# Kernel optimization log

Measured on AMD Instinct MI355X. Metric: run time of the kernel, lower is better.

Reference implementation:

```python
import jax, jax.numpy as jnp
import numpy as np

DIM = 384
HEADS = 12
WIN = (2, 7, 7)
MLP_RATIO = 4.0
EPS = 1e-5


def _rel_index(Wt, Wh, Ww):
    t, h, w = np.meshgrid(np.arange(Wt), np.arange(Wh), np.arange(Ww), indexing='ij')
    coords = np.stack([t, h, w]).reshape(3, -1).T  # (N,3)
    rel = coords[:, None] - coords[None]  # (N,N,3)
    rel[..., 0] += Wt - 1
    rel[..., 1] += Wh - 1
    rel[..., 2] += Ww - 1
    rel[..., 0] *= (2 * Wh - 1) * (2 * Ww - 1)
    rel[..., 1] *= (2 * Ww - 1)
    return rel.sum(-1)  # (N,N) int


def setup_inputs() -> dict:
    key = jax.random.key(0)
    ks = jax.random.split(key, 16)
    d = DIM
    hdim = int(d * MLP_RATIO)
    Wt, Wh, Ww = WIN
    table_size = (2 * Wt - 1) * (2 * Wh - 1) * (2 * Ww - 1)
    s = lambda fan: 1.0 / np.sqrt(fan)
    return {
        'x': jax.random.normal(ks[0], (2, 8, 56, 56, d), jnp.float32),
        'norm1_g': jnp.ones((d,), jnp.float32),
        'norm1_b': jnp.zeros((d,), jnp.float32),
        'qkv_w': jax.random.normal(ks[1], (d, 3 * d), jnp.float32) * s(d),
        'qkv_b': jnp.zeros((3 * d,), jnp.float32),
        'proj_w': jax.random.normal(ks[2], (d, d), jnp.float32) * s(d),
        'proj_b': jnp.zeros((d,), jnp.float32),
        'bias_table': jax.random.normal(ks[3], (table_size, HEADS), jnp.float32) * 0.02,
        'norm2_g': jnp.ones((d,), jnp.float32),
        'norm2_b': jnp.zeros((d,), jnp.float32),
        'fc1_w': jax.random.normal(ks[4], (d, hdim), jnp.float32) * s(d),
        'fc1_b': jnp.zeros((hdim,), jnp.float32),
        'fc2_w': jax.random.normal(ks[5], (hdim, d), jnp.float32) * s(hdim),
        'fc2_b': jnp.zeros((d,), jnp.float32),
        'rel_index': jnp.asarray(_rel_index(*WIN), jnp.int32),
    }


def _ln(x, g, b):
    mu = x.mean(-1, keepdims=True)
    var = ((x - mu) ** 2).mean(-1, keepdims=True)
    return (x - mu) * jax.lax.rsqrt(var + EPS) * g + b


def _window_partition(x, win):
    B, T, H, W, C = x.shape
    Wt, Wh, Ww = win
    x = x.reshape(B, T // Wt, Wt, H // Wh, Wh, W // Ww, Ww, C)
    x = x.transpose(0, 1, 3, 5, 2, 4, 6, 7)
    return x.reshape(-1, Wt * Wh * Ww, C)


def _window_reverse(win_x, win, B, T, H, W):
    Wt, Wh, Ww = win
    C = win_x.shape[-1]
    x = win_x.reshape(B, T // Wt, H // Wh, W // Ww, Wt, Wh, Ww, C)
    x = x.transpose(0, 1, 4, 2, 5, 3, 6, 7)
    return x.reshape(B, T, H, W, C)


def reference(x, norm1_g, norm1_b, qkv_w, qkv_b, proj_w, proj_b, bias_table,
              norm2_g, norm2_b, fc1_w, fc1_b, fc2_w, fc2_b, rel_index):
    B, T, H, W, C = x.shape
    Wt, Wh, Ww = WIN
    N = Wt * Wh * Ww
    shift = (Wt // 2, Wh // 2, Ww // 2)
    head_dim = C // HEADS
    scale = head_dim ** -0.5

    shortcut = x
    h = _ln(x, norm1_g, norm1_b)
    h = jnp.roll(h, shift=(-shift[0], -shift[1], -shift[2]), axis=(1, 2, 3))
    # dims chosen divisible by window -> no padding branch
    wins = _window_partition(h, WIN)  # (BnW, N, C)
    BnW = wins.shape[0]

    qkv = wins @ qkv_w + qkv_b  # (BnW, N, 3C)
    qkv = qkv.reshape(BnW, N, 3, HEADS, head_dim).transpose(2, 0, 3, 1, 4)
    q, k, v = qkv[0] * scale, qkv[1], qkv[2]  # (BnW, H, N, d)

    bias = bias_table[rel_index.reshape(-1)].reshape(N, N, HEADS).transpose(2, 0, 1)
    attn = jnp.einsum('bhnd,bhmd->bhnm', q, k) + bias[None]
    attn = jax.nn.softmax(attn, axis=-1)
    out = jnp.einsum('bhnm,bhmd->bhnd', attn, v)
    out = out.transpose(0, 2, 1, 3).reshape(BnW, N, C)
    out = out @ proj_w + proj_b

    h = _window_reverse(out.reshape(-1, Wt, Wh, Ww, C), WIN, B, T, H, W)
    h = jnp.roll(h, shift=shift, axis=(1, 2, 3))
    x = shortcut + h

    h2 = _ln(x, norm2_g, norm2_b)
    h2 = jax.nn.gelu(h2 @ fc1_w + fc1_b, approximate=False) @ fc2_w + fc2_b
    return x + h2
```

## Files before the change

kernel.cpp:

```cpp
#include <hip/hip_runtime.h>
#include <cstdint>
#include <cstddef>


typedef __bf16 bf16x8 __attribute__((ext_vector_type(8)));
typedef __bf16 bf16x4 __attribute__((ext_vector_type(4)));
typedef float f32x4 __attribute__((ext_vector_type(4)));

#define DIM 384
#define QKV_DIM 1152
#define HID 1536
#define NHEADS 12
#define NTOK 50176
#define NWIN 512

__device__ __forceinline__ void gload16(const void* g, void* s) {
  __builtin_amdgcn_global_load_lds(
      (const __attribute__((address_space(1))) void*)g,
      (__attribute__((address_space(3))) void*)s, 16, 0, 0);
}

__global__ __launch_bounds__(256) void build_tokmap_k(int* __restrict__ map) {
  int t = blockIdx.x * 256 + threadIdx.x;
  if (t >= NTOK) return;
  int win = t / 98, n = t - win * 98;
  int b = win >> 8, tw = (win >> 6) & 3, hw = (win >> 3) & 7, ww = win & 7;
  int dt = n / 49; int rem = n - dt * 49; int dh = rem / 7, dw = rem - dh * 7;
  int t0 = (tw * 2 + dt + 1) & 7;
  int h0 = hw * 7 + dh + 3; if (h0 >= 56) h0 -= 56;
  int w0 = ww * 7 + dw + 3; if (w0 >= 56) w0 -= 56;
  map[t] = ((b * 8 + t0) * 56 + h0) * 56 + w0;
}

__global__ __launch_bounds__(256) void expand_biasp_k(const float* __restrict__ table,
                                                      const int* __restrict__ rel,
                                                      float* __restrict__ out) {
  int e = blockIdx.x * 256 + threadIdx.x;
  if (e >= NHEADS * 49 * 256) return;
  int r = e & 3, l = (e >> 2) & 63;
  int rest = e >> 8;
  int ni = rest % 7, mi = (rest / 7) % 7, h = rest / 49;
  int i = mi * 16 + (l >> 4) * 4 + r;
  int j = ni * 16 + (l & 15);
  float v;
  if (j >= 98) v = -1e30f;
  else if (i >= 98) v = 0.f;
  else v = table[rel[i * 98 + j] * NHEADS + h];
  out[e] = v;
}

__global__ __launch_bounds__(256) void pack_w64_k(const float* __restrict__ W,
                                                  __bf16* __restrict__ WP,
                                                  int K, int N, int nk,
                                                  int scaleCols, float scale) {
  int idx = blockIdx.x * 256 + threadIdx.x;
  if (idx >= (K * N) >> 3) return;
  int l = idx & 63, f = (idx >> 6) & 7;
  int rest = idx >> 9, kt = rest % nk, cn = rest / nk;
  int n = f >> 1, kk = f & 1;
  int col = cn * 64 + n * 16 + (l & 15);
  int k0 = kt * 64 + (kk * 4 + (l >> 4)) * 8;
  float sc = (col < scaleCols) ? scale : 1.0f;
  bf16x8 v;
  #pragma unroll
  for (int j = 0; j < 8; ++j)
    v[j] = (__bf16)(W[(size_t)(k0 + j) * N + col] * sc);
  *(bf16x8*)(WP + (size_t)idx * 8) = v;
}

__global__ __launch_bounds__(256) void scale_bias_k(const float* __restrict__ b,
                                                    float* __restrict__ out,
                                                    int n, int scaleCols, float scale) {
  int e = blockIdx.x * 256 + threadIdx.x;
  if (e >= n) return;
  out[e] = b[e] * (e < scaleCols ? scale : 1.0f);
}

__global__ __launch_bounds__(384) void vtrans_k(const __bf16* __restrict__ qkv,
                                                __bf16* __restrict__ vt) {
  __shared__ __align__(1024) char T[98304];
  int win = blockIdx.x, t = threadIdx.x;
  const __bf16* base = qkv + (size_t)win * 98 * QKV_DIM + 768 + t;
  #pragma unroll
  for (int c = 0; c < 16; ++c) {
    bf16x8 pk;
    #pragma unroll
    for (int e2 = 0; e2 < 8; ++e2) {
      int tok = c * 8 + e2;
      pk[e2] = (tok < 98) ? base[(size_t)tok * QKV_DIM] : (__bf16)0.f;
    }
    *(bf16x8*)(T + t * 256 + ((c ^ (t & 15)) << 4)) = pk;
  }
  __syncthreads();
  char* wb = (char*)(vt + (size_t)win * 49152);
  #pragma unroll
  for (int i = 0; i < 16; ++i) {
    int g = i * 6144 + t * 16;
    int row = g >> 8, p = (g >> 4) & 15;
    bf16x8 v = *(const bf16x8*)(T + row * 256 + (p << 4));
    int lc = p ^ (row & 15);
    *(bf16x8*)(wb + row * 256 + (lc << 4)) = v;
  }
}

template <typename T, bool MAP>
__global__ __launch_bounds__(256) void ln_pack_k(const T* __restrict__ x,
                                                 const float* __restrict__ g,
                                                 const float* __restrict__ bta,
                                                 __bf16* __restrict__ outp,
                                                 const int* __restrict__ map) {
  const int w = threadIdx.x >> 6, l = threadIdx.x & 63;
  const int tok = blockIdx.x * 32 + w * 8 + (l >> 3);
  const int src = MAP ? map[tok] : tok;
  const T* row = x + (size_t)src * DIM;
  const int o0 = l & 7;
  float v[6][8];
  float s = 0.f;
  #pragma unroll
  for (int j = 0; j < 6; ++j) {
    const int c = (o0 + 8 * j) * 8;
    if constexpr (sizeof(T) == 4) {
      f32x4 p0 = *(const f32x4*)(row + c);
      f32x4 p1 = *(const f32x4*)(row + c + 4);
      #pragma unroll
      for (int e = 0; e < 4; ++e) { v[j][e] = p0[e]; v[j][e + 4] = p1[e]; }
    } else {
      bf16x8 p = *(const bf16x8*)(row + c);
      #pragma unroll
      for (int e = 0; e < 8; ++e) v[j][e] = (float)p[e];
    }
    #pragma unroll
    for (int e = 0; e < 8; ++e) s += v[j][e];
  }
  s += __shfl_xor(s, 1, 64); s += __shfl_xor(s, 2, 64); s += __shfl_xor(s, 4, 64);
  const float mu = s * (1.f / DIM);
  float var = 0.f;
  #pragma unroll
  for (int j = 0; j < 6; ++j)
    #pragma unroll
    for (int e = 0; e < 8; ++e) { float d = v[j][e] - mu; var += d * d; }
  var += __shfl_xor(var, 1, 64); var += __shfl_xor(var, 2, 64); var += __shfl_xor(var, 4, 64);
  const float rs = rsqrtf(var * (1.f / DIM) + 1e-5f);
  const int mg = tok >> 6, m = (tok >> 4) & 3, lr = tok & 15;
  const int kk = o0 >> 2, lg = o0 & 3;
  __bf16* dst = outp + (size_t)mg * 24576 + (m * 2 + kk) * 512 + (lg * 16 + lr) * 8;
  #pragma unroll
  for (int j = 0; j < 6; ++j) {
    const int c = (o0 + 8 * j) * 8;
    f32x4 g0 = *(const f32x4*)(g + c), g1 = *(const f32x4*)(g + c + 4);
    f32x4 b0 = *(const f32x4*)(bta + c), b1 = *(const f32x4*)(bta + c + 4);
    bf16x8 ov;
    #pragma unroll
    for (int e = 0; e < 4; ++e) {
      ov[e] = (__bf16)((v[j][e] - mu) * rs * g0[e] + b0[e]);
      ov[e + 4] = (__bf16)((v[j][e + 4] - mu) * rs * g1[e] + b1[e]);
    }
    *(bf16x8*)(dst + (size_t)j * 4096) = ov;
  }
}

template <int EPI, int NK>
__global__ __launch_bounds__(256) void gemm_stream_k(const __bf16* __restrict__ AP,
                                                     const __bf16* __restrict__ WP,
                                                     const float* __restrict__ bias,
                                                     int N,
                                                     __bf16* __restrict__ outb,
                                                     float* __restrict__ outf,
                                                     const __bf16* __restrict__ residb) {
  __shared__ __align__(1024) char lds[32768];
  const int tid = threadIdx.x;
  const int l = tid & 63, w = tid >> 6;
  const int lr = l & 15, lg = l >> 4;
  const int ntile = N >> 6;
  const int nwg = gridDim.x, qd = nwg >> 3, rm = nwg & 7;
  const int xcd = blockIdx.x & 7;
  const int wgid = (xcd < rm ? xcd * (qd + 1) : rm * (qd + 1) + (xcd - rm) * qd)
                   + (blockIdx.x >> 3);
  const int bm = wgid / ntile, bn = wgid - bm * ntile;
  const int mg = bm * 4 + w;
  const int m0 = mg << 6, n0 = bn << 6;
  const __bf16* pA = AP + (size_t)mg * (NK * 4096) + l * 8;
  const __bf16* pB = WP + (size_t)bn * (NK * 4096) + l * 8;

  bf16x8 a[2][8], b[2][8];
  f32x4 acc[4][4] = {};
  #pragma unroll
  for (int f = 0; f < 8; ++f) {
    a[0][f] = *(const bf16x8*)(pA + f * 512);
    b[0][f] = *(const bf16x8*)(pB + f * 512);
  }
  #pragma unroll
  for (int kt = 0; kt < NK; ++kt) {
    const int cur = kt & 1, nxt = cur ^ 1;
    if (kt < NK - 1) {
      const size_t ko = (size_t)(kt + 1) * 4096;
      #pragma unroll
      for (int f = 0; f < 8; ++f) {
        a[nxt][f] = *(const bf16x8*)(pA + ko + f * 512);
        b[nxt][f] = *(const bf16x8*)(pB + ko + f * 512);
      }
      asm volatile("s_waitcnt vmcnt(16)" ::: "memory");
    } else {
      asm volatile("s_waitcnt vmcnt(0)" ::: "memory");
    }
    __builtin_amdgcn_sched_barrier(0);
    __builtin_amdgcn_s_setprio(1);
    #pragma unroll
    for (int kk = 0; kk < 2; ++kk)
      #pragma unroll
      for (int m = 0; m < 4; ++m)
        #pragma unroll
        for (int n = 0; n < 4; ++n)
          acc[m][n] = __builtin_amdgcn_mfma_f32_16x16x32_bf16(
              b[cur][n * 2 + kk], a[cur][m * 2 + kk], acc[m][n], 0, 0, 0);
    __builtin_amdgcn_s_setprio(0);
  }

  char* abuf = lds + (w << 13);
  if (EPI == 3) {
    #pragma unroll
    for (int hh = 0; hh < 2; ++hh) {
      #pragma unroll
      for (int m = 0; m < 4; ++m) {
        const int row = (m << 4) + lr;
        #pragma unroll
        for (int n2 = 0; n2 < 2; ++n2) {
          const int n = (hh << 1) + n2;
          const int gcol = n0 + (n << 4) + (lg << 2);
          f32x4 a4 = acc[m][n] + *(const f32x4*)(bias + gcol);
          const int ch = (n2 << 2) + lg;
          *(f32x4*)(abuf + (row << 7) + ((ch ^ (row & 7)) << 4)) = a4;
        }
      }
      asm volatile("s_waitcnt lgkmcnt(0)" ::: "memory");
      __builtin_amdgcn_sched_barrier(0);
      #pragma unroll
      for (int i = 0; i < 8; ++i) {
        const int row = (i << 3) + (l >> 3);
        const int p = (l & 7) ^ (row & 7);
        f32x4 v = *(const f32x4*)(abuf + (row << 7) + (p << 4));
        const int grow = m0 + row;
        const int gcol = n0 + (hh << 5) + ((l & 7) << 2);
        bf16x4 sv = *(const bf16x4*)(residb + (size_t)grow * N + gcol);
        f32x4 o;
        #pragma unroll
        for (int r = 0; r < 4; ++r) o[r] = v[r] + (float)sv[r];
        *(f32x4*)(outf + (size_t)grow * N + gcol) = o;
      }
      if (hh == 0) {
        asm volatile("s_waitcnt lgkmcnt(0)" ::: "memory");
        __builtin_amdgcn_sched_barrier(0);
      }
    }
  } else {
    #pragma unroll
    for (int m = 0; m < 4; ++m) {
      const int row = (m << 4) + lr;
      #pragma unroll
      for (int n = 0; n < 4; ++n) {
        const int gcol = n0 + (n << 4) + (lg << 2);
        f32x4 a4 = acc[m][n] + *(const f32x4*)(bias + gcol);
        bf16x4 c;
        if (EPI == 4) {
          #pragma unroll
          for (int r = 0; r < 4; ++r) {
            float vv = a4[r];
            float y = vv * (1.0f + 0.044715f * vv * vv);
            c[r] = (__bf16)(vv / (1.0f + __expf(-1.5957691216057308f * y)));
          }
        } else {
          #pragma unroll
          for (int r = 0; r < 4; ++r) c[r] = (__bf16)a4[r];
        }
        const int ch = (n << 1) + (lg >> 1);
        *(bf16x4*)(abuf + (row << 7) + ((ch ^ (row & 7)) << 4) + ((lg & 1) << 3)) = c;
      }
    }
    asm volatile("s_waitcnt lgkmcnt(0)" ::: "memory");
    __builtin_amdgcn_sched_barrier(0);
    if (EPI == 4) {
      #pragma unroll
      for (int f = 0; f < 8; ++f) {
        const int row = ((f >> 1) << 4) + lr;
        const int lc = ((f & 1) << 2) + (l >> 4);
        const int ph = lc ^ (row & 7);
        bf16x8 v = *(const bf16x8*)(abuf + (row << 7) + (ph << 4));
        *(bf16x8*)(outb + ((size_t)(mg * 24 + bn) * 8 + f) * 512 + l * 8) = v;
      }
    } else {
      #pragma unroll
      for (int i = 0; i < 8; ++i) {
        const int row = (i << 3) + (l >> 3);
        const int p = (l & 7) ^ (row & 7);
        bf16x8 v = *(const bf16x8*)(abuf + (row << 7) + (p << 4));
        *(bf16x8*)(outb + (size_t)(m0 + row) * N + n0 + ((l & 7) << 3)) = v;
      }
    }
  }
}

__global__ __launch_bounds__(256) void gemm_proj_k(const __bf16* __restrict__ A,
                                                   const __bf16* __restrict__ WP,
                                                   const float* __restrict__ bias,
                                                   int M, int N, int K,
                                                   __bf16* __restrict__ outb,
                                                   const float* __restrict__ residf,
                                                   const int* __restrict__ tokmap) {
  __shared__ __align__(1024) char lds[32768];
  const int tid = threadIdx.x;
  const int l = tid & 63, w = tid >> 6;
  const int lr = l & 15, lg = l >> 4;
  const int ntile = N >> 6;
  const int nwg = gridDim.x, qd = nwg >> 3, rm = nwg & 7;
  const int xcd = blockIdx.x & 7;
  const int wgid = (xcd < rm ? xcd * (qd + 1) : rm * (qd + 1) + (xcd - rm) * qd)
                   + (blockIdx.x >> 3);
  const int bm = wgid / ntile, bn = wgid - bm * ntile;
  const int m0 = (bm << 8) + (w << 6);
  const int n0 = bn << 6;
  const int nk = K >> 6;
  const int sch = (l & 7) ^ ((l >> 3) & 7);
  const __bf16* pa = A + (size_t)(m0 + (l >> 3)) * K + sch * 8;
  char* abuf = lds + (w << 13);
  const __bf16* pB = WP + (size_t)bn * nk * 4096 + l * 8;

#define STAGEA(kt)                                                   \
  { const size_t ko_ = (size_t)(kt) << 6;                            \
    _Pragma("unroll")                                                \
    for (int s_ = 0; s_ < 8; ++s_)                                   \
      gload16(pa + (size_t)(s_ * 8) * K + ko_, abuf + s_ * 1024); }
#define LOADB(kt)                                                    \
  { const __bf16* p_ = pB + (size_t)(kt) * 4096;                     \
    _Pragma("unroll")                                                \
    for (int f_ = 0; f_ < 8; ++f_)                                   \
      b[f_] = *(const bf16x8*)(p_ + f_ * 512); }
#define LDA()                                                        \
  { _Pragma("unroll")                                                \
    for (int kk_ = 0; kk_ < 2; ++kk_) {                              \
      const int ck_ = (kk_ << 2) + lg;                               \
      _Pragma("unroll")                                              \
      for (int m_ = 0; m_ < 4; ++m_) {                               \
        int r_ = (m_ << 4) + lr;                                     \
        a[m_][kk_] = *(const bf16x8*)(abuf + (r_ << 7) +             \
                                      ((ck_ ^ (r_ & 7)) << 4));      \
      } }                                                            \
    asm volatile("s_waitcnt lgkmcnt(0)" ::: "memory");               \
    __builtin_amdgcn_sched_barrier(0); }

  bf16x8 a[4][2], b[8];
  f32x4 acc[4][4] = {};
  STAGEA(0)
  asm volatile("s_waitcnt vmcnt(0)" ::: "memory");
  LDA()
  for (int kt = 0; kt < nk; ++kt) {
    LOADB(kt)
    const bool pf = (kt + 1 < nk);
    if (pf) STAGEA(kt + 1)
    __builtin_amdgcn_s_setprio(1);
    #pragma unroll
    for (int kk = 0; kk < 2; ++kk)
      #pragma unroll
      for (int m = 0; m < 4; ++m)
        #pragma unroll
        for (int n = 0; n < 4; ++n)
          acc[m][n] = __builtin_amdgcn_mfma_f32_16x16x32_bf16(b[n * 2 + kk], a[m][kk],
                                                              acc[m][n], 0, 0, 0);
    __builtin_amdgcn_s_setprio(0);
    if (pf) {
      asm volatile("s_waitcnt vmcnt(0)" ::: "memory");
      LDA()
    }
  }
#undef STAGEA
#undef LOADB
#undef LDA

  #pragma unroll
  for (int m = 0; m < 4; ++m) {
    const int row = (m << 4) + lr;
    #pragma unroll
    for (int n = 0; n < 4; ++n) {
      const int gcol = n0 + (n << 4) + (lg << 2);
      f32x4 a4 = acc[m][n] + *(const f32x4*)(bias + gcol);
      bf16x4 c;
      #pragma unroll
      for (int r = 0; r < 4; ++r) c[r] = (__bf16)a4[r];
      const int ch = (n << 1) + (lg >> 1);
      *(bf16x4*)(abuf + (row << 7) + ((ch ^ (row & 7)) << 4) + ((lg & 1) << 3)) = c;
    }
  }
  asm volatile("s_waitcnt lgkmcnt(0)" ::: "memory");
  __builtin_amdgcn_sched_barrier(0);
  #pragma unroll
  for (int i = 0; i < 8; ++i) {
    const int row = (i << 3) + (l >> 3);
    const int p = (l & 7) ^ (row & 7);
    bf16x8 v = *(const bf16x8*)(abuf + (row << 7) + (p << 4));
    const int gcol = n0 + ((l & 7) << 3);
    const int dst = tokmap[m0 + row];
    const float* rp = residf + (size_t)dst * N + gcol;
    f32x4 r0 = *(const f32x4*)rp, r1 = *(const f32x4*)(rp + 4);
    bf16x8 c2;
    #pragma unroll
    for (int j = 0; j < 4; ++j) {
      c2[j] = (__bf16)(r0[j] + (float)v[j]);
      c2[j + 4] = (__bf16)(r1[j] + (float)v[j + 4]);
    }
    *(bf16x8*)(outb + (size_t)dst * N + gcol) = c2;
  }
}

__global__ __launch_bounds__(64) void attn_k(const __bf16* __restrict__ qkv,
                                             const __bf16* __restrict__ vt,
                                             const float* __restrict__ pb,
                                             __bf16* __restrict__ out) {
  __shared__ __align__(1024) char P[4096];
  const int l = threadIdx.x, lr = l & 15, lg = l >> 4;
  const int bid = blockIdx.x;
  const int xc = bid & 7, kk = bid >> 3;
  const int wh = (kk / 7) * 8 + xc, mi = kk % 7;
  const int win = wh / NHEADS, h = wh - win * NHEADS;
  const size_t wbase = (size_t)win * 98 * QKV_DIM;
  const __bf16* qb = qkv + wbase + h * 32;
  const __bf16* kb = qb + 384;
  const bf16x8 z8 = {};
  const f32x4 fz = {};

  bf16x8 kf[7];
  #pragma unroll
  for (int ni = 0; ni < 7; ++ni) {
    int tok = ni * 16 + lr;
    kf[ni] = (tok < 98) ? *(const bf16x8*)(kb + (size_t)tok * QKV_DIM + lg * 8) : z8;
  }
  int qt = mi * 16 + lr;
  bf16x8 qf = (qt < 98) ? *(const bf16x8*)(qb + (size_t)qt * QKV_DIM + lg * 8) : z8;
  const f32x4* pbp = (const f32x4*)pb + (size_t)((h * 7 + mi) * 7) * 64 + l;
  f32x4 bv[7];
  #pragma unroll
  for (int ni = 0; ni < 7; ++ni) bv[ni] = pbp[ni * 64];

  f32x4 s[7];
  #pragma unroll
  for (int ni = 0; ni < 7; ++ni)
    s[ni] = __builtin_amdgcn_mfma_f32_16x16x32_bf16(qf, kf[ni], fz, 0, 0, 0);

  if (l < 32) {
    int row = l >> 1, c = 14 + (l & 1);
    *(f32x4*)(P + row * 256 + ((c ^ (row & 7)) << 4)) = fz;
  }

  #pragma unroll
  for (int r = 0; r < 4; ++r) {
    float mx = -1e30f;
    #pragma unroll
    for (int ni = 0; ni < 7; ++ni) {
      float vv = s[ni][r] + bv[ni][r];
      s[ni][r] = vv;
      mx = fmaxf(mx, vv);
    }
    #pragma unroll
    for (int m2 = 1; m2 < 16; m2 <<= 1) mx = fmaxf(mx, __shfl_xor(mx, m2, 64));
    float sum = 0.f;
    #pragma unroll
    for (int ni = 0; ni < 7; ++ni) { float p = __expf(s[ni][r] - mx); s[ni][r] = p; sum += p; }
    #pragma unroll
    for (int m2 = 1; m2 < 16; m2 <<= 1) sum += __shfl_xor(sum, m2, 64);
    float inv = 1.0f / sum;
    int il = lg * 4 + r;
    #pragma unroll
    for (int ni = 0; ni < 7; ++ni) {
      int j = ni * 16 + lr;
      *(__bf16*)(P + il * 256 + (((j >> 3) ^ (il & 7)) << 4) + ((j & 7) << 1)) =
          (__bf16)(s[ni][r] * inv);
    }
  }
  __syncthreads();

  bf16x8 pa[4];
  #pragma unroll
  for (int ks = 0; ks < 4; ++ks) {
    int ck = ks * 4 + lg;
    pa[ks] = *(const bf16x8*)(P + lr * 256 + ((ck ^ (lr & 7)) << 4));
  }
  const __bf16* vrow = vt + ((size_t)wh * 32) * 128;
  f32x4 oo[2];
  #pragma unroll
  for (int nf = 0; nf < 2; ++nf) {
    int d = nf * 16 + lr;
    f32x4 o = fz;
    #pragma unroll
    for (int ks = 0; ks < 4; ++ks) {
      bf16x8 vb = *(const bf16x8*)(vrow + (size_t)d * 128 + ks * 32 + lg * 8);
      o = __builtin_amdgcn_mfma_f32_16x16x32_bf16(pa[ks], vb, o, 0, 0, 0);
    }
    oo[nf] = o;
  }
  #pragma unroll
  for (int nf = 0; nf < 2; ++nf)
    #pragma unroll
    for (int r = 0; r < 4; ++r)
      *(__bf16*)(P + (lg * 4 + r) * 64 + (((nf << 4) + lr) << 1)) = (__bf16)oo[nf][r];
  asm volatile("s_waitcnt lgkmcnt(0)" ::: "memory");
  __builtin_amdgcn_sched_barrier(0);
  {
    const int row = l >> 2;
    bf16x8 v = *(const bf16x8*)(P + row * 64 + ((l & 3) << 4));
    const int tok = mi * 16 + row;
    if (tok < 98)
      *(bf16x8*)(out + ((size_t)win * 98 + tok) * DIM + h * 32 + ((l & 3) << 3)) = v;
  }
}

extern "C" void kernel_launch(void* const* d_in, const int* in_sizes, int n_in,
                              void* d_out, int out_size, void* d_ws, size_t ws_size,
                              hipStream_t stream) {
  const float* x      = (const float*)d_in[0];
  const float* n1g    = (const float*)d_in[1];
  const float* n1b    = (const float*)d_in[2];
  const float* qkv_w  = (const float*)d_in[3];
  const float* qkv_b  = (const float*)d_in[4];
  const float* proj_w = (const float*)d_in[5];
  const float* proj_b = (const float*)d_in[6];
  const float* btab   = (const float*)d_in[7];
  const float* n2g    = (const float*)d_in[8];
  const float* n2b    = (const float*)d_in[9];
  const float* fc1_w  = (const float*)d_in[10];
  const float* fc1_b  = (const float*)d_in[11];
  const float* fc2_w  = (const float*)d_in[12];
  const float* fc2_b  = (const float*)d_in[13];
  const int*   relidx = (const int*)d_in[14];
  float* outp = (float*)d_out;
  (void)in_sizes; (void)n_in; (void)out_size; (void)ws_size;

  char* ws = (char*)d_ws;
  size_t off = 0;
  auto alloc = [&](size_t bytes) {
    char* p = ws + off;
    off = (off + bytes + 255) & ~(size_t)255;
    return p;
  };
  int*    tokmap  = (int*)alloc((size_t)NTOK * 4);
  float*  biasex  = (float*)alloc((size_t)NHEADS * 49 * 256 * 4);
  __bf16* wqkvP   = (__bf16*)alloc((size_t)QKV_DIM * DIM * 2);
  __bf16* wprojP  = (__bf16*)alloc((size_t)DIM * DIM * 2);
  __bf16* wfc1P   = (__bf16*)alloc((size_t)HID * DIM * 2);
  __bf16* wfc2P   = (__bf16*)alloc((size_t)DIM * HID * 2);
  float*  qkvbS   = (float*)alloc((size_t)QKV_DIM * 4);
  __bf16* tokens  = (__bf16*)alloc((size_t)NTOK * DIM * 2);
  __bf16* qkvbuf  = (__bf16*)alloc((size_t)NTOK * HID * 2);
  __bf16* s1      = (__bf16*)alloc((size_t)NTOK * DIM * 2);
  __bf16* tokens2 = (__bf16*)alloc((size_t)NTOK * DIM * 2);
  __bf16* attnout = tokens;
  __bf16* h1P = qkvbuf;
  __bf16* vt = (__bf16*)d_out;

  const float scale = 0.17677669529663687f;

  build_tokmap_k<<<NTOK / 256, 256, 0, stream>>>(tokmap);
  expand_biasp_k<<<(NHEADS * 49 * 256) / 256, 256, 0, stream>>>(btab, relidx, biasex);
  pack_w64_k<<<(DIM * QKV_DIM / 8) / 256, 256, 0, stream>>>(qkv_w, wqkvP, DIM, QKV_DIM, 6, DIM, scale);
  pack_w64_k<<<(DIM * DIM / 8) / 256, 256, 0, stream>>>(proj_w, wprojP, DIM, DIM, 6, 0, 1.0f);
  pack_w64_k<<<(DIM * HID / 8) / 256, 256, 0, stream>>>(fc1_w, wfc1P, DIM, HID, 6, 0, 1.0f);
  pack_w64_k<<<(HID * DIM / 8) / 256, 256, 0, stream>>>(fc2_w, wfc2P, HID, DIM, 24, 0, 1.0f);
  scale_bias_k<<<(QKV_DIM + 255) / 256, 256, 0, stream>>>(qkv_b, qkvbS, QKV_DIM, DIM, scale);

  ln_pack_k<float, true><<<NTOK / 32, 256, 0, stream>>>(x, n1g, n1b, tokens, tokmap);
  gemm_stream_k<0, 6><<<(NTOK / 256) * (QKV_DIM / 64), 256, 0, stream>>>(
      tokens, wqkvP, qkvbS, QKV_DIM, qkvbuf, nullptr, nullptr);
  vtrans_k<<<NWIN, 384, 0, stream>>>(qkvbuf, vt);
  attn_k<<<NWIN * NHEADS * 7, 64, 0, stream>>>(qkvbuf, vt, biasex, attnout);
  gemm_proj_k<<<(NTOK / 256) * (DIM / 64), 256, 0, stream>>>(
      attnout, wprojP, proj_b, NTOK, DIM, DIM, s1, x, tokmap);
  ln_pack_k<__bf16, false><<<NTOK / 32, 256, 0, stream>>>(s1, n2g, n2b, tokens2, nullptr);
  gemm_stream_k<4, 6><<<(NTOK / 256) * (HID / 64), 256, 0, stream>>>(
      tokens2, wfc1P, fc1_b, HID, h1P, nullptr, nullptr);
  gemm_stream_k<3, 24><<<(NTOK / 256) * (DIM / 64), 256, 0, stream>>>(
      h1P, wfc2P, fc2_b, DIM, nullptr, outp, s1);
}
```

Baseline: 455.2 us.

## Fuse fc1, GELU and fc2 into one MLP kernel keeping hidden activations in LDS

Replaces the separate fc1 (with GELU) and fc2 GEMM launches with one kernel per 64-token tile. The kernel loads the normalized tokens into LDS, computes fc1 chunks with GELU into LDS, and accumulates fc2 directly in registers, then adds bias and the residual. The fc2 weights are repacked in a new 96-column layout to match. This removes the round trip of the large hidden activation through global memory. In exchange, weights are read from global memory per tile without LDS staging, the tile is small, and barriers plus higher register and LDS use limit occupancy.

```diff
diff --git a/kernel.cpp b/kernel.cpp
--- a/kernel.cpp
+++ b/kernel.cpp
@@ -68,6 +68,21 @@
   *(bf16x8*)(WP + (size_t)idx * 8) = v;
 }
 
+__global__ __launch_bounds__(256) void pack_w96_k(const float* __restrict__ W,
+                                                  __bf16* __restrict__ WP) {
+  int idx = blockIdx.x * 256 + threadIdx.x;
+  if (idx >= (HID * DIM) >> 3) return;
+  int l = idx & 63, n = (idx >> 6) % 6;
+  int j8 = (idx / 384) % 48, w = idx / 18432;
+  int col = w * 96 + n * 16 + (l & 15);
+  int k0 = j8 * 32 + (l >> 4) * 8;
+  bf16x8 v;
+  #pragma unroll
+  for (int j = 0; j < 8; ++j)
+    v[j] = (__bf16)W[(size_t)(k0 + j) * DIM + col];
+  *(bf16x8*)(WP + (size_t)idx * 8) = v;
+}
+
 __global__ __launch_bounds__(256) void scale_bias_k(const float* __restrict__ b,
                                                     float* __restrict__ out,
                                                     int n, int scaleCols, float scale) {
@@ -164,9 +179,7 @@
                                                      const __bf16* __restrict__ WP,
                                                      const float* __restrict__ bias,
                                                      int N,
-                                                     __bf16* __restrict__ outb,
-                                                     float* __restrict__ outf,
-                                                     const __bf16* __restrict__ residb) {
+                                                     __bf16* __restrict__ outb) {
   __shared__ __align__(1024) char lds[32768];
   const int tid = threadIdx.x;
   const int l = tid & 63, w = tid >> 6;
@@ -217,84 +230,149 @@
   }
 
   char* abuf = lds + (w << 13);
-  if (EPI == 3) {
-    #pragma unroll
-    for (int hh = 0; hh < 2; ++hh) {
-      #pragma unroll
-      for (int m = 0; m < 4; ++m) {
-        const int row = (m << 4) + lr;
-        #pragma unroll
-        for (int n2 = 0; n2 < 2; ++n2) {
-          const int n = (hh << 1) + n2;
-          const int gcol = n0 + (n << 4) + (lg << 2);
-          f32x4 a4 = acc[m][n] + *(const f32x4*)(bias + gcol);
-          const int ch = (n2 << 2) + lg;
-          *(f32x4*)(abuf + (row << 7) + ((ch ^ (row & 7)) << 4)) = a4;
-        }
-      }
-      asm volatile("s_waitcnt lgkmcnt(0)" ::: "memory");
-      __builtin_amdgcn_sched_barrier(0);
-      #pragma unroll
-      for (int i = 0; i < 8; ++i) {
-        const int row = (i << 3) + (l >> 3);
-        const int p = (l & 7) ^ (row & 7);
-        f32x4 v = *(const f32x4*)(abuf + (row << 7) + (p << 4));
-        const int grow = m0 + row;
-        const int gcol = n0 + (hh << 5) + ((l & 7) << 2);
-        bf16x4 sv = *(const bf16x4*)(residb + (size_t)grow * N + gcol);
-        f32x4 o;
-        #pragma unroll
-        for (int r = 0; r < 4; ++r) o[r] = v[r] + (float)sv[r];
-        *(f32x4*)(outf + (size_t)grow * N + gcol) = o;
-      }
-      if (hh == 0) {
-        asm volatile("s_waitcnt lgkmcnt(0)" ::: "memory");
-        __builtin_amdgcn_sched_barrier(0);
-      }
-    }
-  } else {
+  #pragma unroll
+  for (int m = 0; m < 4; ++m) {
+    const int row = (m << 4) + lr;
+    #pragma unroll
+    for (int n = 0; n < 4; ++n) {
+      const int gcol = n0 + (n << 4) + (lg << 2);
+      f32x4 a4 = acc[m][n] + *(const f32x4*)(bias + gcol);
+      bf16x4 c;
+      #pragma unroll
+      for (int r = 0; r < 4; ++r) c[r] = (__bf16)a4[r];
+      const int ch = (n << 1) + (lg >> 1);
+      *(bf16x4*)(abuf + (row << 7) + ((ch ^ (row & 7)) << 4) + ((lg & 1) << 3)) = c;
+    }
+  }
+  asm volatile("s_waitcnt lgkmcnt(0)" ::: "memory");
+  __builtin_amdgcn_sched_barrier(0);
+  #pragma unroll
+  for (int i = 0; i < 8; ++i) {
+    const int row = (i << 3) + (l >> 3);
+    const int p = (l & 7) ^ (row & 7);
+    bf16x8 v = *(const bf16x8*)(abuf + (row << 7) + (p << 4));
+    *(bf16x8*)(outb + (size_t)(m0 + row) * N + n0 + ((l & 7) << 3)) = v;
+  }
+}
+
+__global__ __launch_bounds__(256, 2) void mlp_fused_k(const __bf16* __restrict__ AP,
+                                                      const __bf16* __restrict__ W1P,
+                                                      const float* __restrict__ b1,
+                                                      const __bf16* __restrict__ W2P,
+                                                      const float* __restrict__ b2,
+                                                      const __bf16* __restrict__ s1,
+                                                      float* __restrict__ outp) {
+  __shared__ __align__(1024) char lds[81920];
+  const int tid = threadIdx.x, l = tid & 63, w = tid >> 6;
+  const int lr = l & 15, lg = l >> 4;
+  const int bid = (blockIdx.x & 7) * (gridDim.x >> 3) + (blockIdx.x >> 3);
+  const int tok0 = bid << 6;
+
+  const __bf16* APg = AP + (size_t)bid * 24576;
+  #pragma unroll
+  for (int i = 0; i < 12; ++i) {
+    const int c = w * 12 + i;
+    gload16(APg + c * 512 + l * 8, lds + c * 1024);
+  }
+  asm volatile("s_waitcnt vmcnt(0)" ::: "memory");
+  asm volatile("s_barrier" ::: "memory");
+
+  char* hbase = lds + 49152;
+  const __bf16* W2w = W2P + (size_t)w * 147456 + l * 8;
+  f32x4 acc2[4][6] = {};
+
+  for (int j = 0; j < 6; ++j) {
+    const int g = j * 4 + w;
+    const __bf16* W1g = W1P + (size_t)g * 24576 + l * 8;
+    f32x4 acc1[4][4] = {};
+    #pragma unroll
+    for (int kt = 0; kt < 6; ++kt) {
+      bf16x8 a[4][2], b[8];
+      #pragma unroll
+      for (int f = 0; f < 8; ++f)
+        b[f] = *(const bf16x8*)(W1g + kt * 4096 + f * 512);
+      #pragma unroll
+      for (int m = 0; m < 4; ++m)
+        #pragma unroll
+        for (int kk = 0; kk < 2; ++kk)
+          a[m][kk] = *(const bf16x8*)(lds + (kt * 8 + m * 2 + kk) * 1024 + l * 16);
+      __builtin_amdgcn_s_setprio(1);
+      #pragma unroll
+      for (int kk = 0; kk < 2; ++kk)
+        #pragma unroll
+        for (int m = 0; m < 4; ++m)
+          #pragma unroll
+          for (int n = 0; n < 4; ++n)
+            acc1[m][n] = __builtin_amdgcn_mfma_f32_16x16x32_bf16(
+                b[n * 2 + kk], a[m][kk], acc1[m][n], 0, 0, 0);
+      __builtin_amdgcn_s_setprio(0);
+    }
+    char* hb = hbase + (w << 13);
     #pragma unroll
     for (int m = 0; m < 4; ++m) {
       const int row = (m << 4) + lr;
       #pragma unroll
       for (int n = 0; n < 4; ++n) {
-        const int gcol = n0 + (n << 4) + (lg << 2);
-        f32x4 a4 = acc[m][n] + *(const f32x4*)(bias + gcol);
+        f32x4 a4 = acc1[m][n] + *(const f32x4*)(b1 + g * 64 + (n << 4) + (lg << 2));
         bf16x4 c;
-        if (EPI == 4) {
-          #pragma unroll
-          for (int r = 0; r < 4; ++r) {
-            float vv = a4[r];
-            float y = vv * (1.0f + 0.044715f * vv * vv);
-            c[r] = (__bf16)(vv / (1.0f + __expf(-1.5957691216057308f * y)));
-          }
-        } else {
-          #pragma unroll
-          for (int r = 0; r < 4; ++r) c[r] = (__bf16)a4[r];
+        #pragma unroll
+        for (int r = 0; r < 4; ++r) {
+          float vv = a4[r];
+          float y = vv * (1.0f + 0.044715f * vv * vv);
+          c[r] = (__bf16)(vv / (1.0f + __expf(-1.5957691216057308f * y)));
         }
         const int ch = (n << 1) + (lg >> 1);
-        *(bf16x4*)(abuf + (row << 7) + ((ch ^ (row & 7)) << 4) + ((lg & 1) << 3)) = c;
+        *(bf16x4*)(hb + (row << 7) + ((ch ^ (row & 7)) << 4) + ((lg & 1) << 3)) = c;
       }
     }
     asm volatile("s_waitcnt lgkmcnt(0)" ::: "memory");
     __builtin_amdgcn_sched_barrier(0);
-    if (EPI == 4) {
-      #pragma unroll
-      for (int f = 0; f < 8; ++f) {
-        const int row = ((f >> 1) << 4) + lr;
-        const int lc = ((f & 1) << 2) + (l >> 4);
-        const int ph = lc ^ (row & 7);
-        bf16x8 v = *(const bf16x8*)(abuf + (row << 7) + (ph << 4));
-        *(bf16x8*)(outb + ((size_t)(mg * 24 + bn) * 8 + f) * 512 + l * 8) = v;
-      }
-    } else {
-      #pragma unroll
-      for (int i = 0; i < 8; ++i) {
-        const int row = (i << 3) + (l >> 3);
-        const int p = (l & 7) ^ (row & 7);
-        bf16x8 v = *(const bf16x8*)(abuf + (row << 7) + (p << 4));
-        *(bf16x8*)(outb + (size_t)(m0 + row) * N + n0 + ((l & 7) << 3)) = v;
-      }
+    asm volatile("s_barrier" ::: "memory");
+    #pragma unroll
+    for (int t = 0; t < 4; ++t) {
+      bf16x8 bh[6][2];
+      #pragma unroll
+      for (int q = 0; q < 2; ++q)
+        #pragma unroll
+        for (int n = 0; n < 6; ++n)
+          bh[n][q] = *(const bf16x8*)(W2w + (size_t)((j * 8 + 2 * t + q) * 6 + n) * 512);
+      bf16x8 ah[4][2];
+      const char* ht = hbase + (t << 13);
+      #pragma unroll
+      for (int m = 0; m < 4; ++m)
+        #pragma unroll
+        for (int q = 0; q < 2; ++q) {
+          const int r = (m << 4) + lr, ck = (q << 2) + lg;
+          ah[m][q] = *(const bf16x8*)(ht + (r << 7) + ((ck ^ (r & 7)) << 4));
+        }
+      __builtin_amdgcn_s_setprio(1);
+      #pragma unroll
+      for (int q = 0; q < 2; ++q)
+        #pragma unroll
+        for (int m = 0; m < 4; ++m)
+          #pragma unroll
+          for (int n = 0; n < 6; ++n)
+            acc2[m][n] = __builtin_amdgcn_mfma_f32_16x16x32_bf16(
+                bh[n][q], ah[m][q], acc2[m][n], 0, 0, 0);
+      __builtin_amdgcn_s_setprio(0);
+    }
+    __builtin_amdgcn_sched_barrier(0);
+    asm volatile("s_barrier" ::: "memory");
+  }
+
+  const int col0 = w * 96;
+  #pragma unroll
+  for (int m = 0; m < 4; ++m) {
+    const int grow = tok0 + (m << 4) + lr;
+    #pragma unroll
+    for (int n = 0; n < 6; ++n) {
+      const int gcol = col0 + (n << 4) + (lg << 2);
+      f32x4 a4 = acc2[m][n] + *(const f32x4*)(b2 + gcol);
+      bf16x4 sv = *(const bf16x4*)(s1 + (size_t)grow * DIM + gcol);
+      f32x4 o;
+      #pragma unroll
+      for (int r = 0; r < 4; ++r) o[r] = a4[r] + (float)sv[r];
+      *(f32x4*)(outp + (size_t)grow * DIM + gcol) = o;
     }
   }
 }
@@ -551,7 +629,6 @@
   __bf16* s1      = (__bf16*)alloc((size_t)NTOK * DIM * 2);
   __bf16* tokens2 = (__bf16*)alloc((size_t)NTOK * DIM * 2);
   __bf16* attnout = tokens;
-  __bf16* h1P = qkvbuf;
   __bf16* vt = (__bf16*)d_out;
 
   const float scale = 0.17677669529663687f;
@@ -561,19 +638,17 @@
   pack_w64_k<<<(DIM * QKV_DIM / 8) / 256, 256, 0, stream>>>(qkv_w, wqkvP, DIM, QKV_DIM, 6, DIM, scale);
   pack_w64_k<<<(DIM * DIM / 8) / 256, 256, 0, stream>>>(proj_w, wprojP, DIM, DIM, 6, 0, 1.0f);
   pack_w64_k<<<(DIM * HID / 8) / 256, 256, 0, stream>>>(fc1_w, wfc1P, DIM, HID, 6, 0, 1.0f);
-  pack_w64_k<<<(HID * DIM / 8) / 256, 256, 0, stream>>>(fc2_w, wfc2P, HID, DIM, 24, 0, 1.0f);
+  pack_w96_k<<<(HID * DIM / 8) / 256, 256, 0, stream>>>(fc2_w, wfc2P);
   scale_bias_k<<<(QKV_DIM + 255) / 256, 256, 0, stream>>>(qkv_b, qkvbS, QKV_DIM, DIM, scale);
 
   ln_pack_k<float, true><<<NTOK / 32, 256, 0, stream>>>(x, n1g, n1b, tokens, tokmap);
   gemm_stream_k<0, 6><<<(NTOK / 256) * (QKV_DIM / 64), 256, 0, stream>>>(
-      tokens, wqkvP, qkvbS, QKV_DIM, qkvbuf, nullptr, nullptr);
+      tokens, wqkvP, qkvbS, QKV_DIM, qkvbuf);
   vtrans_k<<<NWIN, 384, 0, stream>>>(qkvbuf, vt);
   attn_k<<<NWIN * NHEADS * 7, 64, 0, stream>>>(qkvbuf, vt, biasex, attnout);
   gemm_proj_k<<<(NTOK / 256) * (DIM / 64), 256, 0, stream>>>(
       attnout, wprojP, proj_b, NTOK, DIM, DIM, s1, x, tokmap);
   ln_pack_k<__bf16, false><<<NTOK / 32, 256, 0, stream>>>(s1, n2g, n2b, tokens2, nullptr);
-  gemm_stream_k<4, 6><<<(NTOK / 256) * (HID / 64), 256, 0, stream>>>(
-      tokens2, wfc1P, fc1_b, HID, h1P, nullptr, nullptr);
-  gemm_stream_k<3, 24><<<(NTOK / 256) * (DIM / 64), 256, 0, stream>>>(
-      h1P, wfc2P, fc2_b, DIM, nullptr, outp, s1);
-}
+  mlp_fused_k<<<NTOK / 64, 256, 0, stream>>>(
+      tokens2, wfc1P, fc1_b, wfc2P, fc2_b, s1, outp);
+}
```

Measured after the change: 451.7 us. Within noise of the previous version (-0.8%).

## Deepen A-operand prefetch in streaming GEMM and use nontemporal epilogue stores

Applied to the files above, without the earlier changes.

The streaming GEMM loop now triple-buffers the A fragments in registers and loads them two k-steps ahead, while B stays one step ahead. Loads are issued after the wait and before the MFMA block instead of before the wait. This aims to hide more global-load latency behind the matrix instructions. It also adds a launch-bounds occupancy hint of 2 and switches epilogue global stores to nontemporal stores to reduce cache pollution. The hand-written vmcnt(16) no longer matches the new issue order, so correctness relies on the compiler inserting its own waits. The extra buffer raises register pressure.

```diff
diff --git a/kernel.cpp b/kernel.cpp
--- a/kernel.cpp
+++ b/kernel.cpp
@@ -160,13 +160,13 @@
 }
 
 template <int EPI, int NK>
-__global__ __launch_bounds__(256) void gemm_stream_k(const __bf16* __restrict__ AP,
-                                                     const __bf16* __restrict__ WP,
-                                                     const float* __restrict__ bias,
-                                                     int N,
-                                                     __bf16* __restrict__ outb,
-                                                     float* __restrict__ outf,
-                                                     const __bf16* __restrict__ residb) {
+__global__ __launch_bounds__(256, 2) void gemm_stream_k(const __bf16* __restrict__ AP,
+                                                        const __bf16* __restrict__ WP,
+                                                        const float* __restrict__ bias,
+                                                        int N,
+                                                        __bf16* __restrict__ outb,
+                                                        float* __restrict__ outf,
+                                                        const __bf16* __restrict__ residb) {
   __shared__ __align__(1024) char lds[32768];
   const int tid = threadIdx.x;
   const int l = tid & 63, w = tid >> 6;
@@ -182,27 +182,35 @@
   const __bf16* pA = AP + (size_t)mg * (NK * 4096) + l * 8;
   const __bf16* pB = WP + (size_t)bn * (NK * 4096) + l * 8;
 
-  bf16x8 a[2][8], b[2][8];
+  bf16x8 a[3][8], b[2][8];
   f32x4 acc[4][4] = {};
-  #pragma unroll
-  for (int f = 0; f < 8; ++f) {
-    a[0][f] = *(const bf16x8*)(pA + f * 512);
-    b[0][f] = *(const bf16x8*)(pB + f * 512);
-  }
+
+#define ISSA(buf, kt)                                                 \
+  { const __bf16* p_ = pA + (size_t)(kt) * 4096;                      \
+    _Pragma("unroll")                                                 \
+    for (int f_ = 0; f_ < 8; ++f_)                                    \
+      a[buf][f_] = *(const bf16x8*)(p_ + f_ * 512); }
+#define ISSB(buf, kt)                                                 \
+  { const __bf16* p_ = pB + (size_t)(kt) * 4096;                      \
+    _Pragma("unroll")                                                 \
+    for (int f_ = 0; f_ < 8; ++f_)                                    \
+      b[buf][f_] = *(const bf16x8*)(p_ + f_ * 512); }
+
+  ISSA(0, 0)
+  ISSB(0, 0)
+  ISSA(1, 1)
+  __builtin_amdgcn_sched_barrier(0);
+
   #pragma unroll
   for (int kt = 0; kt < NK; ++kt) {
-    const int cur = kt & 1, nxt = cur ^ 1;
     if (kt < NK - 1) {
-      const size_t ko = (size_t)(kt + 1) * 4096;
-      #pragma unroll
-      for (int f = 0; f < 8; ++f) {
-        a[nxt][f] = *(const bf16x8*)(pA + ko + f * 512);
-        b[nxt][f] = *(const bf16x8*)(pB + ko + f * 512);
-      }
       asm volatile("s_waitcnt vmcnt(16)" ::: "memory");
     } else {
       asm volatile("s_waitcnt vmcnt(0)" ::: "memory");
     }
+    __builtin_amdgcn_sched_barrier(0);
+    if (kt + 1 < NK) ISSB((kt + 1) & 1, kt + 1)
+    if (kt + 2 < NK) ISSA((kt + 2) % 3, kt + 2)
     __builtin_amdgcn_sched_barrier(0);
     __builtin_amdgcn_s_setprio(1);
     #pragma unroll
@@ -212,9 +220,11 @@
         #pragma unroll
         for (int n = 0; n < 4; ++n)
           acc[m][n] = __builtin_amdgcn_mfma_f32_16x16x32_bf16(
-              b[cur][n * 2 + kk], a[cur][m * 2 + kk], acc[m][n], 0, 0, 0);
+              b[kt & 1][n * 2 + kk], a[kt % 3][m * 2 + kk], acc[m][n], 0, 0, 0);
     __builtin_amdgcn_s_setprio(0);
   }
+#undef ISSA
+#undef ISSB
 
   char* abuf = lds + (w << 13);
   if (EPI == 3) {
@@ -245,7 +255,7 @@
         f32x4 o;
         #pragma unroll
         for (int r = 0; r < 4; ++r) o[r] = v[r] + (float)sv[r];
-        *(f32x4*)(outf + (size_t)grow * N + gcol) = o;
+        __builtin_nontemporal_store(o, (f32x4*)(outf + (size_t)grow * N + gcol));
       }
       if (hh == 0) {
         asm volatile("s_waitcnt lgkmcnt(0)" ::: "memory");
@@ -285,7 +295,8 @@
         const int lc = ((f & 1) << 2) + (l >> 4);
         const int ph = lc ^ (row & 7);
         bf16x8 v = *(const bf16x8*)(abuf + (row << 7) + (ph << 4));
-        *(bf16x8*)(outb + ((size_t)(mg * 24 + bn) * 8 + f) * 512 + l * 8) = v;
+        __builtin_nontemporal_store(
+            v, (bf16x8*)(outb + ((size_t)(mg * 24 + bn) * 8 + f) * 512 + l * 8));
       }
     } else {
       #pragma unroll
@@ -293,7 +304,8 @@
         const int row = (i << 3) + (l >> 3);
         const int p = (l & 7) ^ (row & 7);
         bf16x8 v = *(const bf16x8*)(abuf + (row << 7) + (p << 4));
-        *(bf16x8*)(outb + (size_t)(m0 + row) * N + n0 + ((l & 7) << 3)) = v;
+        __builtin_nontemporal_store(
+            v, (bf16x8*)(outb + (size_t)(m0 + row) * N + n0 + ((l & 7) << 3)));
       }
     }
   }
```

Measured after the change: 470.5 us. 1.03x slower.
